# Optimization experiments

Measured on AMD Instinct MI355X. Metric: run time of the kernel, lower is better.

The kernel has to match this reference:

```python
import jax, jax.numpy as jnp
import numpy as np

D_MODEL, N_EXPERTS, TOP_K, D_FF = 1024, 8, 2, 4096
B, T = 2, 2048


def setup_inputs() -> dict:
    key = jax.random.key(0)
    k1, k2, k3, k4 = jax.random.split(key, 4)
    x = jax.random.normal(k1, (B, T, D_MODEL), dtype=jnp.float32)
    # kaiming-uniform-ish gate init
    bound = np.sqrt(6.0 / D_MODEL)
    gate_w = jax.random.uniform(k2, (D_MODEL, N_EXPERTS), dtype=jnp.float32, minval=-bound, maxval=bound)
    s1 = 1.0 / np.sqrt(D_MODEL)
    s2 = 1.0 / np.sqrt(D_FF)
    w1 = jax.random.normal(k3, (N_EXPERTS, D_MODEL, D_FF), dtype=jnp.float32) * s1
    w2 = jax.random.normal(k4, (N_EXPERTS, D_FF, D_MODEL), dtype=jnp.float32) * s2
    return {"x": x, "gate_w": gate_w, "w1": w1, "w2": w2}


def reference(x, gate_w, w1, w2):
    Bb, Tt, D = x.shape
    E = w1.shape[0]
    # --- router ---
    logits = jnp.einsum('btd,de->bte', x, gate_w)            # (B,T,E)
    top_v, top_i = jax.lax.top_k(logits, TOP_K)               # (B,T,K)
    weights = jax.nn.softmax(top_v, axis=-1)                  # (B,T,K)
    routing_probs = jax.nn.softmax(logits, axis=-1)           # (B,T,E)
    m = routing_probs.mean(axis=(0, 1))                       # (E,)
    aux_loss = (m * m).sum() * E
    # --- dispatch/combine via dense combine matrix ---
    N = Bb * Tt
    flat_x = x.reshape(N, D)
    idx = top_i.reshape(N, TOP_K)
    w = weights.reshape(N, TOP_K)
    # combine[n,e] = sum_k weights[n,k] * [idx[n,k]==e]
    combine = jnp.zeros((N, E), dtype=x.dtype).at[jnp.arange(N)[:, None], idx].add(w)
    # --- experts: Linear -> GELU(exact) -> Linear (HolographicExpert stand-in) ---
    h = jax.nn.gelu(jnp.einsum('nd,edf->enf', flat_x, w1), approximate=False)  # (E,N,ff)
    y = jnp.einsum('enf,efd->end', h, w2)                                       # (E,N,d)
    out = jnp.einsum('ne,end->nd', combine, y).reshape(Bb, Tt, D)
    return out, aux_loss
```

## Files before the change

kernel.cpp:

```cpp
#include <hip/hip_runtime.h>
#include <hip/hip_bf16.h>

#define DM   1024
#define NE   8
#define DFF  4096
#define NTOK 4096

typedef __attribute__((ext_vector_type(8))) short bf16x8;
typedef __attribute__((ext_vector_type(4))) float f32x4;

__device__ __forceinline__ short to_bf16(float f) {
  unsigned u = __float_as_uint(f);
  unsigned r = (u + 0x7fffu + ((u >> 16) & 1u)) >> 16;
  return (short)r;
}

__device__ __forceinline__ void gl16(const void* g, void* l) {
  __builtin_amdgcn_global_load_lds(
      (const __attribute__((address_space(1))) unsigned*)g,
      (__attribute__((address_space(3))) unsigned*)l, 16, 0, 0);
}

__global__ __launch_bounds__(256) void router_kernel(
    const float* __restrict__ x, const float* __restrict__ gw,
    int* __restrict__ cnt, float* __restrict__ psum,
    int* __restrict__ pairs, float* __restrict__ pairW)
{
  __shared__ float gws[DM * NE];
  const int tid = threadIdx.x;
  for (int i = tid * 4; i < DM * NE; i += 256 * 4)
    *reinterpret_cast<float4*>(&gws[i]) = *reinterpret_cast<const float4*>(&gw[i]);
  __syncthreads();

  const int n = blockIdx.x * 256 + tid;
  float acc[NE];
#pragma unroll
  for (int e = 0; e < NE; ++e) acc[e] = 0.f;

  const float4* xr = reinterpret_cast<const float4*>(x + (size_t)n * DM);
  for (int d4 = 0; d4 < DM / 4; ++d4) {
    float4 v = xr[d4];
    const float* gp = &gws[d4 * 4 * NE];
    float xv;
#pragma unroll
    for (int dd = 0; dd < 4; ++dd) {
      xv = (dd == 0) ? v.x : (dd == 1) ? v.y : (dd == 2) ? v.z : v.w;
#pragma unroll
      for (int e = 0; e < NE; ++e) acc[e] = fmaf(xv, gp[dd * NE + e], acc[e]);
    }
  }

  float mx = acc[0];
#pragma unroll
  for (int e = 1; e < NE; ++e) mx = fmaxf(mx, acc[e]);
  float p[NE], s = 0.f;
#pragma unroll
  for (int e = 0; e < NE; ++e) { p[e] = expf(acc[e] - mx); s += p[e]; }
  float inv = 1.f / s;
#pragma unroll
  for (int e = 0; e < NE; ++e) {
    float v = p[e] * inv;
#pragma unroll
    for (int o = 32; o > 0; o >>= 1) v += __shfl_xor(v, o);
    if ((tid & 63) == 0) atomicAdd(&psum[e], v);
  }

  float v0 = -1e30f, v1 = -1e30f; int i0 = 0, i1 = 0;
#pragma unroll
  for (int e = 0; e < NE; ++e) {
    float l = acc[e];
    if (l > v0) { v1 = v0; i1 = i0; v0 = l; i0 = e; }
    else if (l > v1) { v1 = l; i1 = e; }
  }
  float e1 = expf(v1 - v0);
  float den = 1.f + e1;
  pairW[n * 2]     = 1.f / den;
  pairW[n * 2 + 1] = e1 / den;
  int p0 = atomicAdd(&cnt[i0], 1); pairs[i0 * NTOK + p0] = n * 2;
  int p1 = atomicAdd(&cnt[i1], 1); pairs[i1 * NTOK + p1] = n * 2 + 1;
}

__global__ void finalize_kernel(const int* __restrict__ cnt, int* __restrict__ off,
                                const float* __restrict__ psum, float* __restrict__ aux)
{
  if (threadIdx.x == 0 && blockIdx.x == 0) {
    int o = 0;
    for (int e = 0; e < NE; ++e) { off[e] = o; o += cnt[e]; }
    off[NE] = o;
    float a = 0.f;
    for (int e = 0; e < NE; ++e) { float me = psum[e] * (1.f / NTOK); a += me * me; }
    aux[0] = a * (float)NE;
  }
}

__global__ __launch_bounds__(256) void convert_x_kernel(
    const float* __restrict__ x, short* __restrict__ xb)
{
  const int i = (blockIdx.x * 256 + threadIdx.x) * 8;
  float4 a = *reinterpret_cast<const float4*>(&x[i]);
  float4 b = *reinterpret_cast<const float4*>(&x[i + 4]);
  union { short s[8]; bf16x8 v; } p;
  p.s[0]=to_bf16(a.x); p.s[1]=to_bf16(a.y); p.s[2]=to_bf16(a.z); p.s[3]=to_bf16(a.w);
  p.s[4]=to_bf16(b.x); p.s[5]=to_bf16(b.y); p.s[6]=to_bf16(b.z); p.s[7]=to_bf16(b.w);
  *reinterpret_cast<bf16x8*>(&xb[i]) = p.v;
}

__global__ __launch_bounds__(256) void transpose_kernel(
    const float* __restrict__ w1, const float* __restrict__ w2,
    short* __restrict__ w1t, short* __restrict__ w2t)
{
  const int z = blockIdx.z;
  const float* src; short* dst; int R, C, rt, ct;
  if (z < 8) { src = w1 + (size_t)z * DM * DFF; dst = w1t + (size_t)z * DM * DFF;
               R = DM; C = DFF; ct = blockIdx.x; rt = blockIdx.y; }
  else       { src = w2 + (size_t)(z - 8) * DM * DFF; dst = w2t + (size_t)(z - 8) * DM * DFF;
               R = DFF; C = DM; ct = blockIdx.y; rt = blockIdx.x; }
  const int r0 = rt * 64, c0 = ct * 64;
  __shared__ float t[64][65];
  const int tid = threadIdx.x;
  {
    const int row = tid >> 4;
    const int col = (tid & 15) * 4;
#pragma unroll
    for (int it = 0; it < 4; ++it) {
      float4 v = *reinterpret_cast<const float4*>(&src[(size_t)(r0 + it * 16 + row) * C + c0 + col]);
      t[it * 16 + row][col]     = v.x;
      t[it * 16 + row][col + 1] = v.y;
      t[it * 16 + row][col + 2] = v.z;
      t[it * 16 + row][col + 3] = v.w;
    }
  }
  __syncthreads();
  {
    const int oc  = tid >> 3;
    const int orr = (tid & 7) * 8;
#pragma unroll
    for (int it = 0; it < 2; ++it) {
      union { short s[8]; bf16x8 v; } p;
#pragma unroll
      for (int j = 0; j < 8; ++j) p.s[j] = to_bf16(t[orr + j][it * 32 + oc]);
      *reinterpret_cast<bf16x8*>(&dst[(size_t)(c0 + it * 32 + oc) * R + r0 + orr]) = p.v;
    }
  }
}

__global__ __launch_bounds__(256) void gemm1_kernel(
    const short* __restrict__ xb, const short* __restrict__ w1t,
    const int* __restrict__ cnt, const int* __restrict__ off,
    const int* __restrict__ pairs, short* __restrict__ h)
{
  const int wg = (blockIdx.x & 7) * 1024 + (blockIdx.x >> 3);
  const int m0  = (wg & 31) * 128;
  const int e   = (wg >> 5) & 7;
  const int ff0 = (wg >> 8) * 128;
  const int M = cnt[e];
  if (m0 >= M) return;
  const int base = off[e];

  __shared__ __attribute__((aligned(16))) short As[128 * 32];
  __shared__ __attribute__((aligned(16))) short Bs[128 * 32];

  const int tid  = threadIdx.x;
  const int lane = tid & 63;
  const int w    = tid >> 6;
  const int wm = w >> 1, wn = w & 1;

  const int srow0 = (w * 2 + 0) * 16 + (lane >> 2);
  const int srow1 = (w * 2 + 1) * 16 + (lane >> 2);
  const int skoff = (lane & 3) * 8;
  int gi0 = m0 + srow0; if (gi0 > M - 1) gi0 = M - 1;
  int gi1 = m0 + srow1; if (gi1 > M - 1) gi1 = M - 1;
  const int tok0 = pairs[e * NTOK + gi0] >> 1;
  const int tok1 = pairs[e * NTOK + gi1] >> 1;
  const short* ga0 = xb + (size_t)tok0 * DM + skoff;
  const short* ga1 = xb + (size_t)tok1 * DM + skoff;
  const short* gb0 = w1t + ((size_t)e * DFF + ff0 + srow0) * DM + skoff;
  const short* gb1 = w1t + ((size_t)e * DFF + ff0 + srow1) * DM + skoff;
  short* la0 = As + (w * 2 + 0) * 512;
  short* la1 = As + (w * 2 + 1) * 512;
  short* lb0 = Bs + (w * 2 + 0) * 512;
  short* lb1 = Bs + (w * 2 + 1) * 512;

  f32x4 acc[4][4];
#pragma unroll
  for (int i = 0; i < 4; ++i)
#pragma unroll
    for (int j = 0; j < 4; ++j) acc[i][j] = (f32x4){0.f, 0.f, 0.f, 0.f};

  const int lrow = lane & 15;
  const int lk   = (lane >> 4) * 8;

  for (int k0 = 0; k0 < DM; k0 += 32) {
    gl16(ga0 + k0, la0);
    gl16(ga1 + k0, la1);
    gl16(gb0 + k0, lb0);
    gl16(gb1 + k0, lb1);
    __syncthreads();

    bf16x8 af[4], bfv[4];
#pragma unroll
    for (int i = 0; i < 4; ++i)
      af[i] = *reinterpret_cast<const bf16x8*>(&As[(wm * 64 + i * 16 + lrow) * 32 + lk]);
#pragma unroll
    for (int j = 0; j < 4; ++j)
      bfv[j] = *reinterpret_cast<const bf16x8*>(&Bs[(wn * 64 + j * 16 + lrow) * 32 + lk]);
#pragma unroll
    for (int i = 0; i < 4; ++i)
#pragma unroll
      for (int j = 0; j < 4; ++j)
        acc[i][j] = __builtin_amdgcn_mfma_f32_16x16x32_bf16(af[i], bfv[j], acc[i][j], 0, 0, 0);

    __syncthreads();
  }

  const int rbase = wm * 64 + (lane >> 4) * 4;
  const int cb    = ff0 + wn * 64 + (lane & 15);
#pragma unroll
  for (int i = 0; i < 4; ++i) {
#pragma unroll
    for (int r = 0; r < 4; ++r) {
      const int grow = m0 + rbase + i * 16 + r;
      if (grow < M) {
#pragma unroll
        for (int j = 0; j < 4; ++j) {
          float v = acc[i][j][r];
          float g = 0.5f * v * (1.f + erff(v * 0.70710678118f));
          h[(size_t)(base + grow) * DFF + cb + j * 16] = to_bf16(g);
        }
      }
    }
  }
}

__global__ __launch_bounds__(256) void gemm2_kernel(
    const short* __restrict__ h, const short* __restrict__ w2t,
    const int* __restrict__ cnt, const int* __restrict__ off,
    const int* __restrict__ pairs, const float* __restrict__ pairW,
    float* __restrict__ out)
{
  const int wg = (blockIdx.x & 7) * 256 + (blockIdx.x >> 3);
  const int m0 = (wg & 31) * 128;
  const int e  = (wg >> 5) & 7;
  const int d0 = (wg >> 8) * 128;
  const int M = cnt[e];
  if (m0 >= M) return;
  const int base = off[e];

  __shared__ __attribute__((aligned(16))) short As[128 * 32];
  __shared__ __attribute__((aligned(16))) short Bs[128 * 32];

  const int tid  = threadIdx.x;
  const int lane = tid & 63;
  const int w    = tid >> 6;
  const int wm = w >> 1, wn = w & 1;

  const int srow0 = (w * 2 + 0) * 16 + (lane >> 2);
  const int srow1 = (w * 2 + 1) * 16 + (lane >> 2);
  const int skoff = (lane & 3) * 8;
  int gi0 = m0 + srow0; if (gi0 > M - 1) gi0 = M - 1;
  int gi1 = m0 + srow1; if (gi1 > M - 1) gi1 = M - 1;
  const short* ga0 = h + (size_t)(base + gi0) * DFF + skoff;
  const short* ga1 = h + (size_t)(base + gi1) * DFF + skoff;
  const short* gb0 = w2t + ((size_t)e * DM + d0 + srow0) * DFF + skoff;
  const short* gb1 = w2t + ((size_t)e * DM + d0 + srow1) * DFF + skoff;
  short* la0 = As + (w * 2 + 0) * 512;
  short* la1 = As + (w * 2 + 1) * 512;
  short* lb0 = Bs + (w * 2 + 0) * 512;
  short* lb1 = Bs + (w * 2 + 1) * 512;

  f32x4 acc[4][4];
#pragma unroll
  for (int i = 0; i < 4; ++i)
#pragma unroll
    for (int j = 0; j < 4; ++j) acc[i][j] = (f32x4){0.f, 0.f, 0.f, 0.f};

  const int lrow = lane & 15;
  const int lk   = (lane >> 4) * 8;

  for (int k0 = 0; k0 < DFF; k0 += 32) {
    gl16(ga0 + k0, la0);
    gl16(ga1 + k0, la1);
    gl16(gb0 + k0, lb0);
    gl16(gb1 + k0, lb1);
    __syncthreads();

    bf16x8 af[4], bfv[4];
#pragma unroll
    for (int i = 0; i < 4; ++i)
      af[i] = *reinterpret_cast<const bf16x8*>(&As[(wm * 64 + i * 16 + lrow) * 32 + lk]);
#pragma unroll
    for (int j = 0; j < 4; ++j)
      bfv[j] = *reinterpret_cast<const bf16x8*>(&Bs[(wn * 64 + j * 16 + lrow) * 32 + lk]);
#pragma unroll
    for (int i = 0; i < 4; ++i)
#pragma unroll
      for (int j = 0; j < 4; ++j)
        acc[i][j] = __builtin_amdgcn_mfma_f32_16x16x32_bf16(af[i], bfv[j], acc[i][j], 0, 0, 0);

    __syncthreads();
  }

  const int rbase = wm * 64 + (lane >> 4) * 4;
  const int cb    = d0 + wn * 64 + (lane & 15);
#pragma unroll
  for (int i = 0; i < 4; ++i) {
#pragma unroll
    for (int r = 0; r < 4; ++r) {
      const int grow = m0 + rbase + i * 16 + r;
      if (grow < M) {
        const int pr  = pairs[e * NTOK + grow];
        const float wgt = pairW[pr];
        const int tk  = pr >> 1;
#pragma unroll
        for (int j = 0; j < 4; ++j)
          atomicAdd(&out[(size_t)tk * DM + cb + j * 16], wgt * acc[i][j][r]);
      }
    }
  }
}

extern "C" void kernel_launch(void* const* d_in, const int* in_sizes, int n_in,
                              void* d_out, int out_size, void* d_ws, size_t ws_size,
                              hipStream_t stream)
{
  const float* x  = (const float*)d_in[0];
  const float* gw = (const float*)d_in[1];
  const float* w1 = (const float*)d_in[2];
  const float* w2 = (const float*)d_in[3];
  float* outf = (float*)d_out;

  int*   cnt   = (int*)d_ws;
  int*   off   = cnt + 8;
  float* psum  = (float*)(cnt + 20);
  int*   pairs = (int*)((char*)d_ws + 512);
  float* pairW = (float*)((char*)d_ws + 512 + NE * NTOK * 4);
  short* xb    = (short*)((char*)d_ws + (size_t)(1)  * (1 << 20));
  short* w1t   = (short*)((char*)d_ws + (size_t)(16) * (1 << 20));
  short* w2t   = (short*)((char*)d_ws + (size_t)(80) * (1 << 20));
  short* h     = (short*)((char*)d_ws + (size_t)(144)* (1 << 20));

  hipMemsetAsync(d_ws, 0, 512, stream);
  hipMemsetAsync(d_out, 0, (size_t)out_size * sizeof(float), stream);

  router_kernel<<<NTOK / 256, 256, 0, stream>>>(x, gw, cnt, psum, pairs, pairW);
  finalize_kernel<<<1, 64, 0, stream>>>(cnt, off, psum, outf + (size_t)NTOK * DM);
  convert_x_kernel<<<NTOK * DM / (256 * 8), 256, 0, stream>>>(x, xb);
  transpose_kernel<<<dim3(64, 16, 16), 256, 0, stream>>>(w1, w2, w1t, w2t);
  gemm1_kernel<<<8192, 256, 0, stream>>>(xb, w1t, cnt, off, pairs, h);
  gemm2_kernel<<<2048, 256, 0, stream>>>(h, w2t, cnt, off, pairs, pairW, outf);
}
```

Baseline: 461.6 us.

## Use 256x256 tiles with double-buffered swizzled LDS and split-K in expert GEMMs

Both expert GEMMs move from 128x128 tiles with K=32 steps to 256x256 tiles with K=64 steps, 512 threads, and double-buffered LDS staging that prefetches the next K slice during compute. LDS rows are XOR-swizzled to avoid bank conflicts on fragment reads. The second GEMM splits K into two halves whose partial sums are combined through the existing atomic accumulation. This raises arithmetic intensity and overlaps loads with MFMA, at the cost of 128 KB of LDS (one block per CU), high register use, and extra atomics.

```diff
diff --git a/kernel.cpp b/kernel.cpp
--- a/kernel.cpp
+++ b/kernel.cpp
@@ -144,179 +144,203 @@
   }
 }
 
-__global__ __launch_bounds__(256) void gemm1_kernel(
+__global__ __launch_bounds__(512) void gemm1_kernel(
     const short* __restrict__ xb, const short* __restrict__ w1t,
     const int* __restrict__ cnt, const int* __restrict__ off,
     const int* __restrict__ pairs, short* __restrict__ h)
 {
-  const int wg = (blockIdx.x & 7) * 1024 + (blockIdx.x >> 3);
-  const int m0  = (wg & 31) * 128;
-  const int e   = (wg >> 5) & 7;
-  const int ff0 = (wg >> 8) * 128;
-  const int M = cnt[e];
+  const int wg = (blockIdx.x & 7) * 256 + (blockIdx.x >> 3);
+  const int mt = wg & 15;
+  const int e  = (wg >> 4) & 7;
+  const int ft = wg >> 7;
+  const int M  = cnt[e];
+  const int m0 = mt * 256;
   if (m0 >= M) return;
+  const int ff0  = ft * 256;
   const int base = off[e];
 
-  __shared__ __attribute__((aligned(16))) short As[128 * 32];
-  __shared__ __attribute__((aligned(16))) short Bs[128 * 32];
+  __shared__ __attribute__((aligned(16))) short As[2][256 * 64];
+  __shared__ __attribute__((aligned(16))) short Bs[2][256 * 64];
 
   const int tid  = threadIdx.x;
   const int lane = tid & 63;
-  const int w    = tid >> 6;
-  const int wm = w >> 1, wn = w & 1;
-
-  const int srow0 = (w * 2 + 0) * 16 + (lane >> 2);
-  const int srow1 = (w * 2 + 1) * 16 + (lane >> 2);
-  const int skoff = (lane & 3) * 8;
-  int gi0 = m0 + srow0; if (gi0 > M - 1) gi0 = M - 1;
-  int gi1 = m0 + srow1; if (gi1 > M - 1) gi1 = M - 1;
-  const int tok0 = pairs[e * NTOK + gi0] >> 1;
-  const int tok1 = pairs[e * NTOK + gi1] >> 1;
-  const short* ga0 = xb + (size_t)tok0 * DM + skoff;
-  const short* ga1 = xb + (size_t)tok1 * DM + skoff;
-  const short* gb0 = w1t + ((size_t)e * DFF + ff0 + srow0) * DM + skoff;
-  const short* gb1 = w1t + ((size_t)e * DFF + ff0 + srow1) * DM + skoff;
-  short* la0 = As + (w * 2 + 0) * 512;
-  short* la1 = As + (w * 2 + 1) * 512;
-  short* lb0 = Bs + (w * 2 + 0) * 512;
-  short* lb1 = Bs + (w * 2 + 1) * 512;
-
-  f32x4 acc[4][4];
-#pragma unroll
-  for (int i = 0; i < 4; ++i)
+  const int wv   = tid >> 6;
+  const int wm   = wv >> 2;
+  const int wn   = wv & 3;
+
+  const int srow = tid >> 3;
+  const int sswz = ((tid & 7) ^ (srow & 7)) * 8;
+  const short* gA[4]; const short* gB[4];
+#pragma unroll
+  for (int r = 0; r < 4; ++r) {
+    const int row = r * 64 + srow;
+    int gi = m0 + row; if (gi > M - 1) gi = M - 1;
+    const int tok = pairs[e * NTOK + gi] >> 1;
+    gA[r] = xb + (size_t)tok * DM + sswz;
+    gB[r] = w1t + ((size_t)e * DFF + ff0 + row) * DM + sswz;
+  }
+
+#define STAGE1(buf, k0) do { \
+  _Pragma("unroll") for (int r = 0; r < 4; ++r) gl16(gA[r] + (k0), &As[buf][r * 4096 + wv * 512]); \
+  _Pragma("unroll") for (int r = 0; r < 4; ++r) gl16(gB[r] + (k0), &Bs[buf][r * 4096 + wv * 512]); \
+} while (0)
+
+  int cro[2];
+#pragma unroll
+  for (int c = 0; c < 2; ++c)
+    cro[c] = (((c * 4 + (lane >> 4)) ^ (lane & 7)) << 3);
+  const int arow0 = wm * 128 + (lane & 15);
+  const int brow0 = wn * 64  + (lane & 15);
+
+  f32x4 acc[8][4];
+#pragma unroll
+  for (int i = 0; i < 8; ++i)
 #pragma unroll
     for (int j = 0; j < 4; ++j) acc[i][j] = (f32x4){0.f, 0.f, 0.f, 0.f};
 
-  const int lrow = lane & 15;
-  const int lk   = (lane >> 4) * 8;
-
-  for (int k0 = 0; k0 < DM; k0 += 32) {
-    gl16(ga0 + k0, la0);
-    gl16(ga1 + k0, la1);
-    gl16(gb0 + k0, lb0);
-    gl16(gb1 + k0, lb1);
+  STAGE1(0, 0);
+  __syncthreads();
+
+  for (int t = 0; t < 16; ++t) {
+    const int cur = t & 1;
+    if (t < 15) STAGE1(cur ^ 1, (t + 1) * 64);
+#pragma unroll
+    for (int c = 0; c < 2; ++c) {
+      bf16x8 af[8], bfv[4];
+#pragma unroll
+      for (int i = 0; i < 8; ++i)
+        af[i] = *reinterpret_cast<const bf16x8*>(&As[cur][(arow0 + i * 16) * 64 + cro[c]]);
+#pragma unroll
+      for (int j = 0; j < 4; ++j)
+        bfv[j] = *reinterpret_cast<const bf16x8*>(&Bs[cur][(brow0 + j * 16) * 64 + cro[c]]);
+#pragma unroll
+      for (int i = 0; i < 8; ++i)
+#pragma unroll
+        for (int j = 0; j < 4; ++j)
+          acc[i][j] = __builtin_amdgcn_mfma_f32_16x16x32_bf16(af[i], bfv[j], acc[i][j], 0, 0, 0);
+    }
     __syncthreads();
-
-    bf16x8 af[4], bfv[4];
-#pragma unroll
-    for (int i = 0; i < 4; ++i)
-      af[i] = *reinterpret_cast<const bf16x8*>(&As[(wm * 64 + i * 16 + lrow) * 32 + lk]);
-#pragma unroll
-    for (int j = 0; j < 4; ++j)
-      bfv[j] = *reinterpret_cast<const bf16x8*>(&Bs[(wn * 64 + j * 16 + lrow) * 32 + lk]);
-#pragma unroll
-    for (int i = 0; i < 4; ++i)
-#pragma unroll
-      for (int j = 0; j < 4; ++j)
-        acc[i][j] = __builtin_amdgcn_mfma_f32_16x16x32_bf16(af[i], bfv[j], acc[i][j], 0, 0, 0);
-
-    __syncthreads();
-  }
-
-  const int rbase = wm * 64 + (lane >> 4) * 4;
-  const int cb    = ff0 + wn * 64 + (lane & 15);
-#pragma unroll
-  for (int i = 0; i < 4; ++i) {
+  }
+
+  const int erow0 = m0 + wm * 128 + (lane >> 4) * 4;
+  const int ecol0 = ff0 + wn * 64 + (lane & 15);
+#pragma unroll
+  for (int i = 0; i < 8; ++i) {
 #pragma unroll
     for (int r = 0; r < 4; ++r) {
-      const int grow = m0 + rbase + i * 16 + r;
+      const int grow = erow0 + i * 16 + r;
       if (grow < M) {
 #pragma unroll
         for (int j = 0; j < 4; ++j) {
           float v = acc[i][j][r];
           float g = 0.5f * v * (1.f + erff(v * 0.70710678118f));
-          h[(size_t)(base + grow) * DFF + cb + j * 16] = to_bf16(g);
+          h[(size_t)(base + grow) * DFF + ecol0 + j * 16] = to_bf16(g);
         }
       }
     }
   }
-}
-
-__global__ __launch_bounds__(256) void gemm2_kernel(
+#undef STAGE1
+}
+
+__global__ __launch_bounds__(512) void gemm2_kernel(
     const short* __restrict__ h, const short* __restrict__ w2t,
     const int* __restrict__ cnt, const int* __restrict__ off,
     const int* __restrict__ pairs, const float* __restrict__ pairW,
     float* __restrict__ out)
 {
-  const int wg = (blockIdx.x & 7) * 256 + (blockIdx.x >> 3);
-  const int m0 = (wg & 31) * 128;
-  const int e  = (wg >> 5) & 7;
-  const int d0 = (wg >> 8) * 128;
-  const int M = cnt[e];
+  const int wg = (blockIdx.x & 7) * 128 + (blockIdx.x >> 3);
+  const int mt = wg & 15;
+  const int e  = (wg >> 4) & 7;
+  const int z  = wg >> 7;
+  const int dt = z & 3;
+  const int kh = z >> 2;
+  const int M  = cnt[e];
+  const int m0 = mt * 256;
   if (m0 >= M) return;
-  const int base = off[e];
-
-  __shared__ __attribute__((aligned(16))) short As[128 * 32];
-  __shared__ __attribute__((aligned(16))) short Bs[128 * 32];
+  const int d0    = dt * 256;
+  const int kbase = kh * 2048;
+  const int base  = off[e];
+
+  __shared__ __attribute__((aligned(16))) short As[2][256 * 64];
+  __shared__ __attribute__((aligned(16))) short Bs[2][256 * 64];
 
   const int tid  = threadIdx.x;
   const int lane = tid & 63;
-  const int w    = tid >> 6;
-  const int wm = w >> 1, wn = w & 1;
-
-  const int srow0 = (w * 2 + 0) * 16 + (lane >> 2);
-  const int srow1 = (w * 2 + 1) * 16 + (lane >> 2);
-  const int skoff = (lane & 3) * 8;
-  int gi0 = m0 + srow0; if (gi0 > M - 1) gi0 = M - 1;
-  int gi1 = m0 + srow1; if (gi1 > M - 1) gi1 = M - 1;
-  const short* ga0 = h + (size_t)(base + gi0) * DFF + skoff;
-  const short* ga1 = h + (size_t)(base + gi1) * DFF + skoff;
-  const short* gb0 = w2t + ((size_t)e * DM + d0 + srow0) * DFF + skoff;
-  const short* gb1 = w2t + ((size_t)e * DM + d0 + srow1) * DFF + skoff;
-  short* la0 = As + (w * 2 + 0) * 512;
-  short* la1 = As + (w * 2 + 1) * 512;
-  short* lb0 = Bs + (w * 2 + 0) * 512;
-  short* lb1 = Bs + (w * 2 + 1) * 512;
-
-  f32x4 acc[4][4];
-#pragma unroll
-  for (int i = 0; i < 4; ++i)
+  const int wv   = tid >> 6;
+  const int wm   = wv >> 2;
+  const int wn   = wv & 3;
+
+  const int srow = tid >> 3;
+  const int sswz = ((tid & 7) ^ (srow & 7)) * 8;
+  const short* gA[4]; const short* gB[4];
+#pragma unroll
+  for (int r = 0; r < 4; ++r) {
+    const int row = r * 64 + srow;
+    int gi = m0 + row; if (gi > M - 1) gi = M - 1;
+    gA[r] = h + (size_t)(base + gi) * DFF + kbase + sswz;
+    gB[r] = w2t + ((size_t)e * DM + d0 + row) * DFF + kbase + sswz;
+  }
+
+#define STAGE2(buf, k0) do { \
+  _Pragma("unroll") for (int r = 0; r < 4; ++r) gl16(gA[r] + (k0), &As[buf][r * 4096 + wv * 512]); \
+  _Pragma("unroll") for (int r = 0; r < 4; ++r) gl16(gB[r] + (k0), &Bs[buf][r * 4096 + wv * 512]); \
+} while (0)
+
+  int cro[2];
+#pragma unroll
+  for (int c = 0; c < 2; ++c)
+    cro[c] = (((c * 4 + (lane >> 4)) ^ (lane & 7)) << 3);
+  const int arow0 = wm * 128 + (lane & 15);
+  const int brow0 = wn * 64  + (lane & 15);
+
+  f32x4 acc[8][4];
+#pragma unroll
+  for (int i = 0; i < 8; ++i)
 #pragma unroll
     for (int j = 0; j < 4; ++j) acc[i][j] = (f32x4){0.f, 0.f, 0.f, 0.f};
 
-  const int lrow = lane & 15;
-  const int lk   = (lane >> 4) * 8;
-
-  for (int k0 = 0; k0 < DFF; k0 += 32) {
-    gl16(ga0 + k0, la0);
-    gl16(ga1 + k0, la1);
-    gl16(gb0 + k0, lb0);
-    gl16(gb1 + k0, lb1);
+  STAGE2(0, 0);
+  __syncthreads();
+
+  for (int t = 0; t < 32; ++t) {
+    const int cur = t & 1;
+    if (t < 31) STAGE2(cur ^ 1, (t + 1) * 64);
+#pragma unroll
+    for (int c = 0; c < 2; ++c) {
+      bf16x8 af[8], bfv[4];
+#pragma unroll
+      for (int i = 0; i < 8; ++i)
+        af[i] = *reinterpret_cast<const bf16x8*>(&As[cur][(arow0 + i * 16) * 64 + cro[c]]);
+#pragma unroll
+      for (int j = 0; j < 4; ++j)
+        bfv[j] = *reinterpret_cast<const bf16x8*>(&Bs[cur][(brow0 + j * 16) * 64 + cro[c]]);
+#pragma unroll
+      for (int i = 0; i < 8; ++i)
+#pragma unroll
+        for (int j = 0; j < 4; ++j)
+          acc[i][j] = __builtin_amdgcn_mfma_f32_16x16x32_bf16(af[i], bfv[j], acc[i][j], 0, 0, 0);
+    }
     __syncthreads();
-
-    bf16x8 af[4], bfv[4];
-#pragma unroll
-    for (int i = 0; i < 4; ++i)
-      af[i] = *reinterpret_cast<const bf16x8*>(&As[(wm * 64 + i * 16 + lrow) * 32 + lk]);
-#pragma unroll
-    for (int j = 0; j < 4; ++j)
-      bfv[j] = *reinterpret_cast<const bf16x8*>(&Bs[(wn * 64 + j * 16 + lrow) * 32 + lk]);
-#pragma unroll
-    for (int i = 0; i < 4; ++i)
-#pragma unroll
-      for (int j = 0; j < 4; ++j)
-        acc[i][j] = __builtin_amdgcn_mfma_f32_16x16x32_bf16(af[i], bfv[j], acc[i][j], 0, 0, 0);
-
-    __syncthreads();
-  }
-
-  const int rbase = wm * 64 + (lane >> 4) * 4;
-  const int cb    = d0 + wn * 64 + (lane & 15);
-#pragma unroll
-  for (int i = 0; i < 4; ++i) {
+  }
+
+  const int erow0 = m0 + wm * 128 + (lane >> 4) * 4;
+  const int ecol0 = d0 + wn * 64 + (lane & 15);
+#pragma unroll
+  for (int i = 0; i < 8; ++i) {
 #pragma unroll
     for (int r = 0; r < 4; ++r) {
-      const int grow = m0 + rbase + i * 16 + r;
+      const int grow = erow0 + i * 16 + r;
       if (grow < M) {
-        const int pr  = pairs[e * NTOK + grow];
+        const int pr    = pairs[e * NTOK + grow];
         const float wgt = pairW[pr];
-        const int tk  = pr >> 1;
+        const int tok   = pr >> 1;
 #pragma unroll
         for (int j = 0; j < 4; ++j)
-          atomicAdd(&out[(size_t)tk * DM + cb + j * 16], wgt * acc[i][j][r]);
+          atomicAdd(&out[(size_t)tok * DM + ecol0 + j * 16], wgt * acc[i][j][r]);
       }
     }
   }
+#undef STAGE2
 }
 
 extern "C" void kernel_launch(void* const* d_in, const int* in_sizes, int n_in,
@@ -346,6 +370,6 @@
   finalize_kernel<<<1, 64, 0, stream>>>(cnt, off, psum, outf + (size_t)NTOK * DM);
   convert_x_kernel<<<NTOK * DM / (256 * 8), 256, 0, stream>>>(x, xb);
   transpose_kernel<<<dim3(64, 16, 16), 256, 0, stream>>>(w1, w2, w1t, w2t);
-  gemm1_kernel<<<8192, 256, 0, stream>>>(xb, w1t, cnt, off, pairs, h);
-  gemm2_kernel<<<2048, 256, 0, stream>>>(h, w2t, cnt, off, pairs, pairW, outf);
-}
+  gemm1_kernel<<<2048, 512, 0, stream>>>(xb, w1t, cnt, off, pairs, h);
+  gemm2_kernel<<<1024, 512, 0, stream>>>(h, w2t, cnt, off, pairs, pairW, outf);
+}
```

Measured after the change: 529.8 us. 1.15x slower.
